# Kernel optimization log

Hardware: AMD Instinct MI355X
Metric: run time of the kernel (lower is better)

Reference implementation:

```python
import jax, jax.numpy as jnp
import numpy as np

N = 100000   # nodes
E = 1600000  # edges
G = 2048     # graphs in batch
NF = 64      # node_feature_dim
D = 32       # hidden dim (hard-coded in module)
SF = 512     # solvent_feature_dim
BN_EPS = 1e-5


def setup_inputs() -> dict:
    key = jax.random.key(0)
    ks = jax.random.split(key, 24)
    s = 0.1
    return {
        "x": jax.random.normal(ks[0], (N, NF), jnp.float32),
        "edge_index": jax.random.randint(ks[1], (2, E), 0, N, dtype=jnp.int64),
        "batch": jnp.sort(jax.random.randint(ks[2], (N,), 0, G, dtype=jnp.int64)),
        "solvent_fingerprint": jax.random.uniform(ks[3], (G, SF), jnp.float32),
        # GIN layer 1 first Linear (NF->D); layers 2-5 first Linear stacked (D->D)
        "w1a": jax.random.normal(ks[4], (NF, D), jnp.float32) * s,
        "b1a": jnp.zeros((D,), jnp.float32),
        "ws_a": jax.random.normal(ks[5], (4, D, D), jnp.float32) * s,
        "bs_a": jnp.zeros((4, D), jnp.float32),
        # second Linear of all 5 GIN MLPs
        "ws_b": jax.random.normal(ks[6], (5, D, D), jnp.float32) * s,
        "bs_b": jnp.zeros((5, D), jnp.float32),
        # BatchNorm affine params per layer
        "bn_g": jnp.ones((5, D), jnp.float32),
        "bn_b": jnp.zeros((5, D), jnp.float32),
        # dense head
        "fcg_w": jax.random.normal(ks[7], (D, 128), jnp.float32) * s,
        "fcg_b": jnp.zeros((128,), jnp.float32),
        "fs1_w": jax.random.normal(ks[8], (SF, 256), jnp.float32) * s,
        "fs1_b": jnp.zeros((256,), jnp.float32),
        "fs2_w": jax.random.normal(ks[9], (256, 128), jnp.float32) * s,
        "fs2_b": jnp.zeros((128,), jnp.float32),
        "fc1_w": jax.random.normal(ks[10], (256, 1024), jnp.float32) * s,
        "fc1_b": jnp.zeros((1024,), jnp.float32),
        "fc2_w": jax.random.normal(ks[11], (1024, 256), jnp.float32) * s,
        "fc2_b": jnp.zeros((256,), jnp.float32),
        "out_w": jax.random.normal(ks[12], (256, 1), jnp.float32) * s,
        "out_b": jnp.zeros((1,), jnp.float32),
    }


def _bn_relu(h, g, b):
    # BatchNorm1d training-mode math (biased batch variance), then ReLU
    mu = h.mean(axis=0)
    var = h.var(axis=0)
    return jax.nn.relu((h - mu) * jax.lax.rsqrt(var + BN_EPS) * g + b)


def reference(x, edge_index, batch, solvent_fingerprint,
              w1a, b1a, ws_a, bs_a, ws_b, bs_b, bn_g, bn_b,
              fcg_w, fcg_b, fs1_w, fs1_b, fs2_w, fs2_b,
              fc1_w, fc1_b, fc2_w, fc2_b, out_w, out_b):
    src, dst = edge_index[0], edge_index[1]

    def gin_agg(h):
        # GINConv with eps=0: (1+eps)*x_i + sum_{j->i} x_j
        return h + jax.ops.segment_sum(h[src], dst, num_segments=N)

    # layer 1 (NF -> D)
    h = gin_agg(x)
    h = jax.nn.relu(h @ w1a + b1a) @ ws_b[0] + bs_b[0]
    h = _bn_relu(h, bn_g[0], bn_b[0])
    # layers 2-5 (D -> D)
    for i in range(4):
        h = gin_agg(h)
        h = jax.nn.relu(h @ ws_a[i] + bs_a[i]) @ ws_b[i + 1] + bs_b[i + 1]
        h = _bn_relu(h, bn_g[i + 1], bn_b[i + 1])

    pooled = jax.ops.segment_sum(h, batch, num_segments=G)  # [G, D]
    gfeat = jax.nn.relu(pooled @ fcg_w + fcg_b)             # dropout inactive (eval)

    sf = solvent_fingerprint.reshape(-1, SF)
    s = jax.nn.relu(sf @ fs1_w + fs1_b)
    s = jax.nn.relu(s @ fs2_w + fs2_b)

    z = jnp.concatenate([gfeat, s], axis=1)                 # [G, 256]
    z = jax.nn.relu(z @ fc1_w + fc1_b)
    z = jax.nn.relu(z @ fc2_w + fc2_b)
    return z @ out_w + out_b                                # [G, 1]
```

## Files before the change

### kernel.cpp

```cpp
#include <hip/hip_runtime.h>
#include <hip/hip_bf16.h>

static constexpr int N_NODES = 100000;
static constexpr int N_EDGES = 1600000;
static constexpr int N_GRAPH = 2048;
static constexpr float BN_EPS_C = 1e-5f;

static constexpr int BUCK_SHIFT = 9;
static constexpr int NB_BUCK = (N_NODES + 511) >> 9;
static constexpr int PART_B = 256;
static constexpr int CHUNK = N_EDGES / PART_B;
static constexpr int NTOT = NB_BUCK * PART_B;
static constexpr int NSLOT = 8;

typedef unsigned int uint;
typedef unsigned short ushort;


__device__ inline uint pk2(float a, float b) {
    uint ua = __float_as_uint(a), ub = __float_as_uint(b);
    ua = (ua + 0x7fffu + ((ua >> 16) & 1u)) >> 16;
    ub = (ub + 0x7fffu + ((ub >> 16) & 1u)) >> 16;
    return ua | (ub << 16);
}
__device__ inline float b2f_lo(uint u) { return __uint_as_float(u << 16); }
__device__ inline float b2f_hi(uint u) { return __uint_as_float(u & 0xffff0000u); }

__device__ inline void unpack8(uint4 v, float* f) {
    f[0] = b2f_lo(v.x); f[1] = b2f_hi(v.x);
    f[2] = b2f_lo(v.y); f[3] = b2f_hi(v.y);
    f[4] = b2f_lo(v.z); f[5] = b2f_hi(v.z);
    f[6] = b2f_lo(v.w); f[7] = b2f_hi(v.w);
}


__global__ __launch_bounds__(256) void k_bcount(const int* __restrict__ dst, int* __restrict__ cnt) {
    __shared__ int h[NB_BUCK];
    int blk = blockIdx.x, tid = threadIdx.x;
    for (int i = tid; i < NB_BUCK; i += 256) h[i] = 0;
    __syncthreads();
    int base = blk * CHUNK;
    for (int e = base + tid; e < base + CHUNK; e += 256) {
        int d = __builtin_nontemporal_load(&dst[e]);
        atomicAdd(&h[d >> BUCK_SHIFT], 1);
    }
    __syncthreads();
    for (int i = tid; i < NB_BUCK; i += 256) cnt[i * PART_B + blk] = h[i];
}

__global__ __launch_bounds__(256) void k_scan_partial2(const int* __restrict__ v, int* __restrict__ part, int n) {
    __shared__ int sw[4];
    int b = blockIdx.x, tid = threadIdx.x;
    int base = b * 1024;
    int s = 0;
#pragma unroll
    for (int r = 0; r < 4; ++r) {
        int i = base + r * 256 + tid;
        if (i < n) s += v[i];
    }
#pragma unroll
    for (int off = 32; off > 0; off >>= 1) s += __shfl_down(s, off);
    if ((tid & 63) == 0) sw[tid >> 6] = s;
    __syncthreads();
    if (tid == 0) part[b] = sw[0] + sw[1] + sw[2] + sw[3];
}

__global__ __launch_bounds__(256) void k_scan_offsets2(int* __restrict__ part, int nb, int* __restrict__ bstart) {
    __shared__ int sh[256];
    int tid = threadIdx.x;
    sh[tid] = (tid < nb) ? part[tid] : 0;
    __syncthreads();
    if (tid == 0) {
        int run = 0;
        for (int i = 0; i < nb; ++i) { int v = sh[i]; sh[i] = run; run += v; }
        bstart[NB_BUCK] = run;
    }
    __syncthreads();
    if (tid < nb) part[tid] = sh[tid];
}

__global__ __launch_bounds__(256) void k_scan_final2(int* __restrict__ cnt, const int* __restrict__ part,
                                                     int* __restrict__ bstart, int n) {
    __shared__ int wsum[4];
    int b = blockIdx.x, tid = threadIdx.x;
    int lane = tid & 63, w = tid >> 6;
    int base = b * 1024 + tid * 4;
    int v[4];
#pragma unroll
    for (int r = 0; r < 4; ++r) {
        int i = base + r;
        v[r] = (i < n) ? cnt[i] : 0;
    }
    int tsum = v[0] + v[1] + v[2] + v[3];
    int inc = tsum;
#pragma unroll
    for (int off = 1; off < 64; off <<= 1) {
        int t = __shfl_up(inc, off);
        if (lane >= off) inc += t;
    }
    if (lane == 63) wsum[w] = inc;
    __syncthreads();
    int woff = 0;
    for (int ww = 0; ww < w; ++ww) woff += wsum[ww];
    int run = part[b] + woff + (inc - tsum);
#pragma unroll
    for (int r = 0; r < 4; ++r) {
        int idx = base + r;
        if (idx < n) {
            int c = v[r];
            cnt[idx] = run;
            if ((idx & (PART_B - 1)) == 0) bstart[idx / PART_B] = run;
            run += c;
        }
    }
}

__global__ __launch_bounds__(256) void k_bpart(const int* __restrict__ src, const int* __restrict__ dst,
                                               const int* __restrict__ cnt, int2* __restrict__ ebuf) {
    __shared__ int cur[NB_BUCK];
    int blk = blockIdx.x, tid = threadIdx.x;
    for (int i = tid; i < NB_BUCK; i += 256) cur[i] = cnt[i * PART_B + blk];
    __syncthreads();
    int base = blk * CHUNK;
    for (int e = base + tid; e < base + CHUNK; e += 256) {
        int d = __builtin_nontemporal_load(&dst[e]);
        int s = __builtin_nontemporal_load(&src[e]);
        int p = atomicAdd(&cur[d >> BUCK_SHIFT], 1);
        ebuf[p] = make_int2(d, s);
    }
}

__global__ __launch_bounds__(256) void k_bfine(const int2* __restrict__ ebuf, const int* __restrict__ bstart,
                                               int* __restrict__ row_ptr, int* __restrict__ row_end,
                                               int* __restrict__ ssrc) {
    __shared__ int fh[512];
    __shared__ int wsum[4];
    int b = blockIdx.x, tid = threadIdx.x;
    int n0 = b << BUCK_SHIFT;
    int e0 = bstart[b], e1 = bstart[b + 1];
    fh[tid] = 0; fh[tid + 256] = 0;
    __syncthreads();
    for (int e = e0 + tid; e < e1; e += 256)
        atomicAdd(&fh[ebuf[e].x - n0], 1);
    __syncthreads();
    int a0 = fh[2 * tid], a1 = fh[2 * tid + 1];
    int s = a0 + a1;
    int lane = tid & 63, w = tid >> 6;
    int inc = s;
#pragma unroll
    for (int off = 1; off < 64; off <<= 1) {
        int t = __shfl_up(inc, off);
        if (lane >= off) inc += t;
    }
    if (lane == 63) wsum[w] = inc;
    __syncthreads();
    int woff = 0;
    for (int ww = 0; ww < w; ++ww) woff += wsum[ww];
    int excl = woff + inc - s;
    int p0 = excl, p1 = excl + a0;
    int node0 = n0 + 2 * tid, node1 = node0 + 1;
    if (node0 < N_NODES) { row_ptr[node0] = e0 + p0; row_end[node0] = e0 + p0 + a0; }
    if (node1 < N_NODES) { row_ptr[node1] = e0 + p1; row_end[node1] = e0 + p1 + a1; }
    fh[2 * tid] = p0; fh[2 * tid + 1] = p1;
    __syncthreads();
    for (int e = e0 + tid; e < e1; e += 256) {
        int2 v = ebuf[e];
        int p = atomicAdd(&fh[v.x - n0], 1);
        ssrc[e0 + p] = v.y;
    }
}


__global__ __launch_bounds__(256) void k_xw1(const float* __restrict__ x, const float* __restrict__ Wa,
                                             ushort* __restrict__ y) {
    __shared__ float sWa[2048];
    int tid = threadIdx.x;
    for (int i = tid; i < 2048; i += 256) {
        int r = i >> 5, c = i & 31;
        sWa[(r << 5) + (c ^ (((r >> 4) & 3) << 2))] = Wa[i];
    }
    __syncthreads();
    int idx = blockIdx.x * 256 + tid;
    int node = idx >> 2;
    int sl = idx & 3;
    int k0 = sl * 16;
    bool active = node < N_NODES;

    float xv[16];
    if (active) {
        const float* xr = x + (size_t)node * 64 + k0;
        *(float4*)(xv + 0)  = *(const float4*)(xr + 0);
        *(float4*)(xv + 4)  = *(const float4*)(xr + 4);
        *(float4*)(xv + 8)  = *(const float4*)(xr + 8);
        *(float4*)(xv + 12) = *(const float4*)(xr + 12);
    } else {
#pragma unroll
        for (int j = 0; j < 16; ++j) xv[j] = 0.f;
    }

    float pj[32];
#pragma unroll
    for (int j = 0; j < 32; ++j) pj[j] = 0.f;
    int sw = sl << 2;
#pragma unroll
    for (int kk = 0; kk < 16; ++kk) {
        float a = xv[kk];
        const float* rb = sWa + ((k0 + kk) << 5);
#pragma unroll
        for (int j4 = 0; j4 < 8; ++j4) {
            int jo = j4 << 2;
            float4 wv = *(const float4*)(rb + (jo ^ sw));
            pj[jo + 0] = fmaf(a, wv.x, pj[jo + 0]);
            pj[jo + 1] = fmaf(a, wv.y, pj[jo + 1]);
            pj[jo + 2] = fmaf(a, wv.z, pj[jo + 2]);
            pj[jo + 3] = fmaf(a, wv.w, pj[jo + 3]);
        }
    }
#pragma unroll
    for (int j = 0; j < 32; ++j) {
        pj[j] += __shfl_xor(pj[j], 1);
        pj[j] += __shfl_xor(pj[j], 2);
    }
    if (active && sl == 0) {
        uint pk[16];
#pragma unroll
        for (int j = 0; j < 16; ++j) pk[j] = pk2(pj[2 * j], pj[2 * j + 1]);
        uint4* yp = (uint4*)(y + (size_t)node * 32);
        yp[0] = make_uint4(pk[0], pk[1], pk[2], pk[3]);
        yp[1] = make_uint4(pk[4], pk[5], pk[6], pk[7]);
        yp[2] = make_uint4(pk[8], pk[9], pk[10], pk[11]);
        yp[3] = make_uint4(pk[12], pk[13], pk[14], pk[15]);
    }
}


__global__ __launch_bounds__(256) void k_fused1y(const ushort* __restrict__ y,
                                                 const int* __restrict__ row_ptr, const int* __restrict__ row_end,
                                                 const int* __restrict__ ssrc,
                                                 const float* __restrict__ ba,
                                                 const float* __restrict__ Wb, const float* __restrict__ bb,
                                                 ushort* __restrict__ uout, float* __restrict__ stats_out) {
    __shared__ float sWb[1024];
    __shared__ float sba[32];
    __shared__ float sbb[32];
    __shared__ float bstats[64];
    __shared__ float tile[64][36];
    int tid = threadIdx.x;
    for (int i = tid; i < 1024; i += 256) sWb[i] = Wb[i];
    if (tid < 32) { sba[tid] = ba[tid]; sbb[tid] = bb[tid]; }
    if (tid < 64) bstats[tid] = 0.f;
    __syncthreads();

    int idx = blockIdx.x * 256 + tid;
    int node = idx >> 2;
    int sl = idx & 3;
    int f8 = sl * 8;
    int nloc = tid >> 2;
    bool active = node < N_NODES;

    float acc[8] = {0.f, 0.f, 0.f, 0.f, 0.f, 0.f, 0.f, 0.f};
    if (active) {
        unpack8(*(const uint4*)(y + (size_t)node * 32 + f8), acc);
        int e = row_ptr[node], e1 = row_end[node];
        float v[8];
        for (; e + 4 <= e1; e += 4) {
            int s0 = ssrc[e], s1 = ssrc[e + 1], s2 = ssrc[e + 2], s3 = ssrc[e + 3];
            uint4 va = *(const uint4*)(y + (size_t)s0 * 32 + f8);
            uint4 vb = *(const uint4*)(y + (size_t)s1 * 32 + f8);
            uint4 vc = *(const uint4*)(y + (size_t)s2 * 32 + f8);
            uint4 vd = *(const uint4*)(y + (size_t)s3 * 32 + f8);
            unpack8(va, v);
#pragma unroll
            for (int j = 0; j < 8; ++j) acc[j] += v[j];
            unpack8(vb, v);
#pragma unroll
            for (int j = 0; j < 8; ++j) acc[j] += v[j];
            unpack8(vc, v);
#pragma unroll
            for (int j = 0; j < 8; ++j) acc[j] += v[j];
            unpack8(vd, v);
#pragma unroll
            for (int j = 0; j < 8; ++j) acc[j] += v[j];
        }
        for (; e < e1; ++e) {
            int s = ssrc[e];
            unpack8(*(const uint4*)(y + (size_t)s * 32 + f8), v);
#pragma unroll
            for (int j = 0; j < 8; ++j) acc[j] += v[j];
        }
    }

    float h8[8];
#pragma unroll
    for (int j = 0; j < 8; ++j) h8[j] = fmaxf(acc[j] + sba[f8 + j], 0.f);
    *(float4*)&tile[nloc][f8] = make_float4(h8[0], h8[1], h8[2], h8[3]);
    *(float4*)&tile[nloc][f8 + 4] = make_float4(h8[4], h8[5], h8[6], h8[7]);
    __syncthreads();

    float uu[8];
#pragma unroll
    for (int j = 0; j < 8; ++j) uu[j] = sbb[f8 + j];
#pragma unroll
    for (int k4 = 0; k4 < 8; ++k4) {
        float4 hv = *(const float4*)&tile[nloc][k4 * 4];
        float hvv[4] = {hv.x, hv.y, hv.z, hv.w};
#pragma unroll
        for (int m = 0; m < 4; ++m) {
            int k = k4 * 4 + m;
            float a = hvv[m];
            const float4* wr = (const float4*)(sWb + k * 32 + f8);
            float4 w0 = wr[0], w1 = wr[1];
            uu[0] = fmaf(a, w0.x, uu[0]);
            uu[1] = fmaf(a, w0.y, uu[1]);
            uu[2] = fmaf(a, w0.z, uu[2]);
            uu[3] = fmaf(a, w0.w, uu[3]);
            uu[4] = fmaf(a, w1.x, uu[4]);
            uu[5] = fmaf(a, w1.y, uu[5]);
            uu[6] = fmaf(a, w1.z, uu[6]);
            uu[7] = fmaf(a, w1.w, uu[7]);
        }
    }

    if (active) {
        uint4 pkv = make_uint4(pk2(uu[0], uu[1]), pk2(uu[2], uu[3]), pk2(uu[4], uu[5]), pk2(uu[6], uu[7]));
        *(uint4*)(uout + (size_t)node * 32 + f8) = pkv;
    } else {
#pragma unroll
        for (int j = 0; j < 8; ++j) uu[j] = 0.f;
    }

#pragma unroll
    for (int j = 0; j < 8; ++j) {
        float v = uu[j];
        float v2 = v * v;
        v += __shfl_xor(v, 4);  v2 += __shfl_xor(v2, 4);
        v += __shfl_xor(v, 8);  v2 += __shfl_xor(v2, 8);
        v += __shfl_xor(v, 16); v2 += __shfl_xor(v2, 16);
        v += __shfl_xor(v, 32); v2 += __shfl_xor(v2, 32);
        if ((tid & 63) < 4) {
            atomicAdd(&bstats[f8 + j], v);
            atomicAdd(&bstats[32 + f8 + j], v2);
        }
    }
    __syncthreads();
    if (tid < 64) atomicAdd(&stats_out[(blockIdx.x & (NSLOT - 1)) * 64 + tid], bstats[tid]);
}


__global__ __launch_bounds__(256) void k_fused(const ushort* __restrict__ uin, ushort* __restrict__ uout,
                                               const float* __restrict__ stats_in, float* __restrict__ stats_out,
                                               const float* __restrict__ bng, const float* __restrict__ bnb,
                                               const int* __restrict__ row_ptr, const int* __restrict__ row_end,
                                               const int* __restrict__ ssrc,
                                               const float* __restrict__ Wa, const float* __restrict__ ba,
                                               const float* __restrict__ Wb, const float* __restrict__ bb) {
    __shared__ float sWa[1024];
    __shared__ float sWb[1024];
    __shared__ float sba[32];
    __shared__ float sbb[32];
    __shared__ float bstats[64];
    int tid = threadIdx.x;
    for (int i = tid; i < 1024; i += 256) {
        int r = i >> 5, c = i & 31;
        sWa[(r << 5) + (c ^ (((r >> 3) & 3) << 2))] = Wa[i];
        sWb[i] = Wb[i];
    }
    if (tid < 32) { sba[tid] = ba[tid]; sbb[tid] = bb[tid]; }
    if (tid < 64) bstats[tid] = 0.f;
    __syncthreads();

    int idx = blockIdx.x * 256 + tid;
    int node = idx >> 2;
    int sl = idx & 3;
    int f8 = sl * 8;
    bool active = node < N_NODES;

    const float inv = 1.0f / (float)N_NODES;
    float sc[8], sh[8];
    {
        float s1[8] = {0,0,0,0,0,0,0,0}, s2[8] = {0,0,0,0,0,0,0,0};
        for (int s = 0; s < NSLOT; ++s) {
            const float* sp = stats_in + s * 64;
            float4 a = *(const float4*)(sp + f8);
            float4 b = *(const float4*)(sp + f8 + 4);
            float4 c = *(const float4*)(sp + 32 + f8);
            float4 d = *(const float4*)(sp + 36 + f8);
            s1[0] += a.x; s1[1] += a.y; s1[2] += a.z; s1[3] += a.w;
            s1[4] += b.x; s1[5] += b.y; s1[6] += b.z; s1[7] += b.w;
            s2[0] += c.x; s2[1] += c.y; s2[2] += c.z; s2[3] += c.w;
            s2[4] += d.x; s2[5] += d.y; s2[6] += d.z; s2[7] += d.w;
        }
        float g[8], b[8];
        *(float4*)g = *(const float4*)(bng + f8); *(float4*)(g + 4) = *(const float4*)(bng + f8 + 4);
        *(float4*)b = *(const float4*)(bnb + f8); *(float4*)(b + 4) = *(const float4*)(bnb + f8 + 4);
#pragma unroll
        for (int j = 0; j < 8; ++j) {
            float mu = s1[j] * inv;
            sc[j] = rsqrtf(s2[j] * inv - mu * mu + BN_EPS_C) * g[j];
            sh[j] = b[j] - mu * sc[j];
        }
    }

    float acc[8] = {0.f, 0.f, 0.f, 0.f, 0.f, 0.f, 0.f, 0.f};
    if (active) {
        float v[8];
        unpack8(*(const uint4*)(uin + (size_t)node * 32 + f8), v);
#pragma unroll
        for (int j = 0; j < 8; ++j) acc[j] = fmaxf(fmaf(v[j], sc[j], sh[j]), 0.f);
        int e = row_ptr[node], e1 = row_end[node];
        for (; e + 4 <= e1; e += 4) {
            int s0 = ssrc[e], s1 = ssrc[e + 1], s2 = ssrc[e + 2], s3 = ssrc[e + 3];
            uint4 va = *(const uint4*)(uin + (size_t)s0 * 32 + f8);
            uint4 vb = *(const uint4*)(uin + (size_t)s1 * 32 + f8);
            uint4 vc = *(const uint4*)(uin + (size_t)s2 * 32 + f8);
            uint4 vd = *(const uint4*)(uin + (size_t)s3 * 32 + f8);
            unpack8(va, v);
#pragma unroll
            for (int j = 0; j < 8; ++j) acc[j] += fmaxf(fmaf(v[j], sc[j], sh[j]), 0.f);
            unpack8(vb, v);
#pragma unroll
            for (int j = 0; j < 8; ++j) acc[j] += fmaxf(fmaf(v[j], sc[j], sh[j]), 0.f);
            unpack8(vc, v);
#pragma unroll
            for (int j = 0; j < 8; ++j) acc[j] += fmaxf(fmaf(v[j], sc[j], sh[j]), 0.f);
            unpack8(vd, v);
#pragma unroll
            for (int j = 0; j < 8; ++j) acc[j] += fmaxf(fmaf(v[j], sc[j], sh[j]), 0.f);
        }
        for (; e < e1; ++e) {
            int s = ssrc[e];
            unpack8(*(const uint4*)(uin + (size_t)s * 32 + f8), v);
#pragma unroll
            for (int j = 0; j < 8; ++j) acc[j] += fmaxf(fmaf(v[j], sc[j], sh[j]), 0.f);
        }
    }

    float pj[32];
#pragma unroll
    for (int j = 0; j < 32; ++j) pj[j] = 0.f;
    int sw = sl << 2;
#pragma unroll
    for (int kk = 0; kk < 8; ++kk) {
        float a = acc[kk];
        const float* rb = sWa + ((f8 + kk) << 5);
#pragma unroll
        for (int j4 = 0; j4 < 8; ++j4) {
            int jo = j4 << 2;
            float4 wv = *(const float4*)(rb + (jo ^ sw));
            pj[jo + 0] = fmaf(a, wv.x, pj[jo + 0]);
            pj[jo + 1] = fmaf(a, wv.y, pj[jo + 1]);
            pj[jo + 2] = fmaf(a, wv.z, pj[jo + 2]);
            pj[jo + 3] = fmaf(a, wv.w, pj[jo + 3]);
        }
    }
#pragma unroll
    for (int j = 0; j < 32; ++j) {
        pj[j] += __shfl_xor(pj[j], 1);
        pj[j] += __shfl_xor(pj[j], 2);
        pj[j] = fmaxf(pj[j] + sba[j], 0.f);
    }

    float uu[8];
#pragma unroll
    for (int j = 0; j < 8; ++j) uu[j] = sbb[f8 + j];
#pragma unroll
    for (int k = 0; k < 32; ++k) {
        float a = pj[k];
        const float4* wr = (const float4*)(sWb + k * 32 + f8);
        float4 w0 = wr[0], w1 = wr[1];
        uu[0] = fmaf(a, w0.x, uu[0]);
        uu[1] = fmaf(a, w0.y, uu[1]);
        uu[2] = fmaf(a, w0.z, uu[2]);
        uu[3] = fmaf(a, w0.w, uu[3]);
        uu[4] = fmaf(a, w1.x, uu[4]);
        uu[5] = fmaf(a, w1.y, uu[5]);
        uu[6] = fmaf(a, w1.z, uu[6]);
        uu[7] = fmaf(a, w1.w, uu[7]);
    }

    if (active) {
        uint4 pkv = make_uint4(pk2(uu[0], uu[1]), pk2(uu[2], uu[3]), pk2(uu[4], uu[5]), pk2(uu[6], uu[7]));
        *(uint4*)(uout + (size_t)node * 32 + f8) = pkv;
    } else {
#pragma unroll
        for (int j = 0; j < 8; ++j) uu[j] = 0.f;
    }

#pragma unroll
    for (int j = 0; j < 8; ++j) {
        float v = uu[j];
        float v2 = v * v;
        v += __shfl_xor(v, 4);  v2 += __shfl_xor(v2, 4);
        v += __shfl_xor(v, 8);  v2 += __shfl_xor(v2, 8);
        v += __shfl_xor(v, 16); v2 += __shfl_xor(v2, 16);
        v += __shfl_xor(v, 32); v2 += __shfl_xor(v2, 32);
        if ((tid & 63) < 4) {
            atomicAdd(&bstats[f8 + j], v);
            atomicAdd(&bstats[32 + f8 + j], v2);
        }
    }
    __syncthreads();
    if (tid < 64) atomicAdd(&stats_out[(blockIdx.x & (NSLOT - 1)) * 64 + tid], bstats[tid]);
}


__global__ __launch_bounds__(256) void k_bn_pool(const ushort* __restrict__ u, const float* __restrict__ stats,
                                                 const float* __restrict__ bng, const float* __restrict__ bnb,
                                                 const int* __restrict__ batch, float* __restrict__ pooled) {
    const int CH = 128;
    int wid = (blockIdx.x * 256 + threadIdx.x) >> 6;
    int lane = threadIdx.x & 63;
    int f = lane & 31, par = lane >> 5;
    int n0 = wid * CH;
    if (n0 >= N_NODES) return;
    int n1 = n0 + CH; if (n1 > N_NODES) n1 = N_NODES;
    const float inv = 1.0f / (float)N_NODES;
    float sv = 0.f, sq = 0.f;
    for (int s = 0; s < NSLOT; ++s) { sv += stats[s * 64 + f]; sq += stats[s * 64 + 32 + f]; }
    float mu = sv * inv;
    float var = sq * inv - mu * mu;
    float sc = rsqrtf(var + BN_EPS_C) * bng[f];
    float sh = bnb[f] - mu * sc;
    float acc = 0.f;
    int curg = -1;
    for (int n = n0 + par; n < n1; n += 2) {
        int g = batch[n];
        if (g != curg) {
            if (curg >= 0) atomicAdd(&pooled[(size_t)curg * 32 + f], acc);
            acc = 0.f; curg = g;
        }
        float v = b2f_lo((uint)u[(size_t)n * 32 + f]);
        acc += fmaxf(fmaf(v, sc, sh), 0.f);
    }
    if (curg >= 0) atomicAdd(&pooled[(size_t)curg * 32 + f], acc);
}


#define GEMM_COMPUTE_16()                                                      \
    _Pragma("unroll")                                                          \
    for (int k = 0; k < 16; ++k) {                                             \
        float4 a4 = *(const float4*)&As[k][ty * 4];                            \
        float4 b4 = *(const float4*)&Bs[k][tx * 4];                            \
        acc[0][0] = fmaf(a4.x, b4.x, acc[0][0]);                               \
        acc[0][1] = fmaf(a4.x, b4.y, acc[0][1]);                               \
        acc[0][2] = fmaf(a4.x, b4.z, acc[0][2]);                               \
        acc[0][3] = fmaf(a4.x, b4.w, acc[0][3]);                               \
        acc[1][0] = fmaf(a4.y, b4.x, acc[1][0]);                               \
        acc[1][1] = fmaf(a4.y, b4.y, acc[1][1]);                               \
        acc[1][2] = fmaf(a4.y, b4.z, acc[1][2]);                               \
        acc[1][3] = fmaf(a4.y, b4.w, acc[1][3]);                               \
        acc[2][0] = fmaf(a4.z, b4.x, acc[2][0]);                               \
        acc[2][1] = fmaf(a4.z, b4.y, acc[2][1]);                               \
        acc[2][2] = fmaf(a4.z, b4.z, acc[2][2]);                               \
        acc[2][3] = fmaf(a4.z, b4.w, acc[2][3]);                               \
        acc[3][0] = fmaf(a4.w, b4.x, acc[3][0]);                               \
        acc[3][1] = fmaf(a4.w, b4.y, acc[3][1]);                               \
        acc[3][2] = fmaf(a4.w, b4.z, acc[3][2]);                               \
        acc[3][3] = fmaf(a4.w, b4.w, acc[3][3]);                               \
    }

__global__ __launch_bounds__(256) void k_gemm_f(const float* __restrict__ A, const float* __restrict__ B,
                                                const float* __restrict__ bias, float* __restrict__ C,
                                                int Nc, int K, int ldc, int do_relu) {
    __shared__ float As[16][64];
    __shared__ float Bs[16][64];
    int tid = threadIdx.x;
    int tx = tid & 15, ty = tid >> 4;
    int bm = blockIdx.x * 64, bn = blockIdx.y * 64;
    float acc[4][4] = {{0.f}};
    int am = tid >> 2;
    int ak = (tid & 3) * 4;
    int bk = tid >> 4;
    int bn4 = (tid & 15) * 4;
    const float* Ap = A + (size_t)(bm + am) * K + ak;
    const float* Bp = B + (size_t)bk * Nc + bn + bn4;
    float4 av = *(const float4*)Ap;
    float4 bv = *(const float4*)Bp;
    for (int k0 = 0; k0 < K; k0 += 16) {
        As[ak + 0][am] = av.x;
        As[ak + 1][am] = av.y;
        As[ak + 2][am] = av.z;
        As[ak + 3][am] = av.w;
        *(float4*)&Bs[bk][bn4] = bv;
        __syncthreads();
        if (k0 + 16 < K) {
            av = *(const float4*)(Ap + k0 + 16);
            bv = *(const float4*)(Bp + (size_t)(k0 + 16) * Nc);
        }
        GEMM_COMPUTE_16()
        __syncthreads();
    }
    float4 bi = *(const float4*)(bias + bn + tx * 4);
#pragma unroll
    for (int i = 0; i < 4; ++i) {
        float4 v;
        v.x = acc[i][0] + bi.x;
        v.y = acc[i][1] + bi.y;
        v.z = acc[i][2] + bi.z;
        v.w = acc[i][3] + bi.w;
        if (do_relu) {
            v.x = fmaxf(v.x, 0.f); v.y = fmaxf(v.y, 0.f);
            v.z = fmaxf(v.z, 0.f); v.w = fmaxf(v.w, 0.f);
        }
        *(float4*)(C + (size_t)(bm + ty * 4 + i) * ldc + bn + tx * 4) = v;
    }
}

__global__ __launch_bounds__(256) void k_gemm_p(const float* __restrict__ A, const float* __restrict__ B,
                                                float* __restrict__ psum, int Nc, int Ktot, int klen) {
    __shared__ float As[16][64];
    __shared__ float Bs[16][64];
    int tid = threadIdx.x;
    int tx = tid & 15, ty = tid >> 4;
    int bm = blockIdx.x * 64, bn = blockIdx.y * 64;
    int kb = blockIdx.z * klen;
    float acc[4][4] = {{0.f}};
    int am = tid >> 2;
    int ak = (tid & 3) * 4;
    int bk = tid >> 4;
    int bn4 = (tid & 15) * 4;
    const float* Ap = A + (size_t)(bm + am) * Ktot + kb + ak;
    const float* Bp = B + (size_t)(kb + bk) * Nc + bn + bn4;
    float4 av = *(const float4*)Ap;
    float4 bv = *(const float4*)Bp;
    for (int k0 = 0; k0 < klen; k0 += 16) {
        As[ak + 0][am] = av.x;
        As[ak + 1][am] = av.y;
        As[ak + 2][am] = av.z;
        As[ak + 3][am] = av.w;
        *(float4*)&Bs[bk][bn4] = bv;
        __syncthreads();
        if (k0 + 16 < klen) {
            av = *(const float4*)(Ap + k0 + 16);
            bv = *(const float4*)(Bp + (size_t)(k0 + 16) * Nc);
        }
        GEMM_COMPUTE_16()
        __syncthreads();
    }
    float* out = psum + (size_t)blockIdx.z * N_GRAPH * Nc;
#pragma unroll
    for (int i = 0; i < 4; ++i) {
        float4 v = make_float4(acc[i][0], acc[i][1], acc[i][2], acc[i][3]);
        *(float4*)(out + (size_t)(bm + ty * 4 + i) * Nc + bn + tx * 4) = v;
    }
}

__global__ __launch_bounds__(256) void k_reduce(const float* __restrict__ psum, const float* __restrict__ bias,
                                                float* __restrict__ C, int S, int Nc, int ldc, int do_relu) {
    int idx = blockIdx.x * 256 + threadIdx.x;
    int nq = Nc >> 2;
    if (idx >= N_GRAPH * nq) return;
    int m = idx / nq;
    int j = (idx - m * nq) * 4;
    float4 s = *(const float4*)(psum + (size_t)m * Nc + j);
    for (int z = 1; z < S; ++z) {
        float4 t = *(const float4*)(psum + (size_t)z * N_GRAPH * Nc + (size_t)m * Nc + j);
        s.x += t.x; s.y += t.y; s.z += t.z; s.w += t.w;
    }
    float4 bi = *(const float4*)(bias + j);
    s.x += bi.x; s.y += bi.y; s.z += bi.z; s.w += bi.w;
    if (do_relu) {
        s.x = fmaxf(s.x, 0.f); s.y = fmaxf(s.y, 0.f);
        s.z = fmaxf(s.z, 0.f); s.w = fmaxf(s.w, 0.f);
    }
    *(float4*)(C + (size_t)m * ldc + j) = s;
}


__global__ __launch_bounds__(256) void k_out(const float* __restrict__ z2, const float* __restrict__ w,
                                             const float* __restrict__ b, float* __restrict__ out) {
    int gid = blockIdx.x * 256 + threadIdx.x;
    int g = gid >> 6;
    int lane = threadIdx.x & 63;
    if (g >= N_GRAPH) return;
    float4 a = *(const float4*)(z2 + (size_t)g * 256 + lane * 4);
    float4 wv = *(const float4*)(w + lane * 4);
    float v = a.x * wv.x + a.y * wv.y + a.z * wv.z + a.w * wv.w;
#pragma unroll
    for (int off = 32; off > 0; off >>= 1) v += __shfl_down(v, off);
    if (lane == 0) out[g] = v + b[0];
}


extern "C" void kernel_launch(void* const* d_in, const int* in_sizes, int n_in,
                              void* d_out, int out_size, void* d_ws, size_t ws_size,
                              hipStream_t stream) {
    const float* x     = (const float*)d_in[0];
    const int*   eidx  = (const int*)d_in[1];
    const int*   batch = (const int*)d_in[2];
    const float* sf    = (const float*)d_in[3];
    const float* w1a   = (const float*)d_in[4];
    const float* b1a   = (const float*)d_in[5];
    const float* ws_a  = (const float*)d_in[6];
    const float* bs_a  = (const float*)d_in[7];
    const float* ws_b  = (const float*)d_in[8];
    const float* bs_b  = (const float*)d_in[9];
    const float* bn_g  = (const float*)d_in[10];
    const float* bn_b  = (const float*)d_in[11];
    const float* fcg_w = (const float*)d_in[12];
    const float* fcg_b = (const float*)d_in[13];
    const float* fs1_w = (const float*)d_in[14];
    const float* fs1_b = (const float*)d_in[15];
    const float* fs2_w = (const float*)d_in[16];
    const float* fs2_b = (const float*)d_in[17];
    const float* fc1_w = (const float*)d_in[18];
    const float* fc1_b = (const float*)d_in[19];
    const float* fc2_w = (const float*)d_in[20];
    const float* fc2_b = (const float*)d_in[21];
    const float* out_w = (const float*)d_in[22];
    const float* out_b = (const float*)d_in[23];
    float* dout = (float*)d_out;

    char* p = (char*)d_ws;
    float*  scr     = (float*)p;  p += (size_t)N_NODES * 64 * 4;
    ushort* u0      = (ushort*)p; p += (size_t)N_NODES * 32 * 2;
    ushort* u1      = (ushort*)p; p += (size_t)N_NODES * 32 * 2;
    int*    ssrc    = (int*)p;    p += (size_t)N_EDGES * 4;
    int*    row_ptr = (int*)p;    p += (size_t)N_NODES * 4;
    int*    row_end = (int*)p;    p += (size_t)N_NODES * 4;
    int*    cnt     = (int*)p;    p += (size_t)NTOT * 4;
    int*    part2   = (int*)p;    p += 512 * 4;
    int*    bstart  = (int*)p;    p += 256 * 4;
    float*  stats   = (float*)p;  p += (size_t)5 * NSLOT * 64 * 4;
    float*  pooled  = (float*)p;  p += (size_t)N_GRAPH * 32 * 4;
    ushort* ybuf    = (ushort*)p; p += (size_t)N_NODES * 32 * 2;

    int2* ebuf = (int2*)scr;

    float* zcat  = scr;
    float* z1buf = zcat + 2048 * 256;
    float* z2buf = z1buf + 2048 * 1024;
    float* s1buf = z2buf + 2048 * 256;
    float* psum  = s1buf + 2048 * 256;

    size_t zero_bytes = ((size_t)5 * NSLOT * 64 + (size_t)N_GRAPH * 32) * 4;
    hipMemsetAsync(stats, 0, zero_bytes, stream);

    const int* esrc = eidx;
    const int* edst = eidx + N_EDGES;

    const int scan_blocks = NTOT / 1024;
    k_bcount<<<PART_B, 256, 0, stream>>>(edst, cnt);
    k_scan_partial2<<<scan_blocks, 256, 0, stream>>>(cnt, part2, NTOT);
    k_scan_offsets2<<<1, 256, 0, stream>>>(part2, scan_blocks, bstart);
    k_scan_final2<<<scan_blocks, 256, 0, stream>>>(cnt, part2, bstart, NTOT);
    k_bpart<<<PART_B, 256, 0, stream>>>(esrc, edst, cnt, ebuf);
    k_bfine<<<NB_BUCK, 256, 0, stream>>>(ebuf, bstart, row_ptr, row_end, ssrc);

    const int SLOT_STRIDE = NSLOT * 64;
    const int nblk4 = (N_NODES * 4 + 255) / 256;

    k_xw1<<<nblk4, 256, 0, stream>>>(x, w1a, ybuf);
    k_fused1y<<<nblk4, 256, 0, stream>>>(ybuf, row_ptr, row_end, ssrc,
                                         b1a, ws_b, bs_b, u0, stats);

    ushort* uin = u0;
    ushort* uout = u1;
    for (int L = 1; L <= 4; ++L) {
        k_fused<<<nblk4, 256, 0, stream>>>(
            uin, uout,
            stats + (size_t)(L - 1) * SLOT_STRIDE, stats + (size_t)L * SLOT_STRIDE,
            bn_g + (L - 1) * 32, bn_b + (L - 1) * 32,
            row_ptr, row_end, ssrc,
            ws_a + (size_t)(L - 1) * 1024, bs_a + (L - 1) * 32,
            ws_b + (size_t)L * 1024, bs_b + L * 32);
        ushort* t = uin; uin = uout; uout = t;
    }

    {
        int waves = (N_NODES + 127) / 128;
        int blocks = (waves + 3) / 4;
        k_bn_pool<<<blocks, 256, 0, stream>>>(uin, stats + (size_t)4 * SLOT_STRIDE,
                                              bn_g + 128, bn_b + 128, batch, pooled);
    }

    k_gemm_f<<<dim3(32, 2), 256, 0, stream>>>(pooled, fcg_w, fcg_b, zcat, 128, 32, 256, 1);
    k_gemm_p<<<dim3(32, 4, 4), 256, 0, stream>>>(sf, fs1_w, psum, 256, 512, 128);
    k_reduce<<<512, 256, 0, stream>>>(psum, fs1_b, s1buf, 4, 256, 256, 1);
    k_gemm_p<<<dim3(32, 2, 4), 256, 0, stream>>>(s1buf, fs2_w, psum, 128, 256, 64);
    k_reduce<<<256, 256, 0, stream>>>(psum, fs2_b, zcat + 128, 4, 128, 256, 1);
    k_gemm_f<<<dim3(32, 16), 256, 0, stream>>>(zcat, fc1_w, fc1_b, z1buf, 1024, 256, 1024, 1);
    k_gemm_p<<<dim3(32, 4, 4), 256, 0, stream>>>(z1buf, fc2_w, psum, 256, 1024, 256);
    k_reduce<<<512, 256, 0, stream>>>(psum, fc2_b, z2buf, 4, 256, 256, 1);
    k_out<<<512, 256, 0, stream>>>(z2buf, out_w, out_b, dout);
}
```

Baseline: 525.0 us.

## Reorder nodes by in-degree within buckets to balance wavefront gather work

Builds, inside each 512-node bucket, a permutation that sorts nodes by in-degree using a small 64-bin histogram and scan. The fused GIN aggregation kernels then process nodes in permuted order, so nodes with similar degree share a wavefront and divergence in the edge loop drops. The cost is an extra perm lookup per node and less coalesced access to the self and output rows, since neighbouring threads now touch scattered nodes within the bucket.

```diff
diff --git a/kernel.cpp b/kernel.cpp
--- a/kernel.cpp
+++ b/kernel.cpp
@@ -132,18 +132,25 @@
 
 __global__ __launch_bounds__(256) void k_bfine(const int2* __restrict__ ebuf, const int* __restrict__ bstart,
                                                int* __restrict__ row_ptr, int* __restrict__ row_end,
-                                               int* __restrict__ ssrc) {
+                                               int* __restrict__ ssrc, int* __restrict__ perm) {
     __shared__ int fh[512];
     __shared__ int wsum[4];
+    __shared__ int dh[64];
+    __shared__ int dcur[64];
     int b = blockIdx.x, tid = threadIdx.x;
     int n0 = b << BUCK_SHIFT;
     int e0 = bstart[b], e1 = bstart[b + 1];
     fh[tid] = 0; fh[tid + 256] = 0;
+    if (tid < 64) dh[tid] = 0;
     __syncthreads();
     for (int e = e0 + tid; e < e1; e += 256)
         atomicAdd(&fh[ebuf[e].x - n0], 1);
     __syncthreads();
     int a0 = fh[2 * tid], a1 = fh[2 * tid + 1];
+    int node0 = n0 + 2 * tid, node1 = node0 + 1;
+    int b0 = a0 < 63 ? a0 : 63, b1 = a1 < 63 ? a1 : 63;
+    if (node0 < N_NODES) atomicAdd(&dh[b0], 1);
+    if (node1 < N_NODES) atomicAdd(&dh[b1], 1);
     int s = a0 + a1;
     int lane = tid & 63, w = tid >> 6;
     int inc = s;
@@ -154,15 +161,26 @@
     }
     if (lane == 63) wsum[w] = inc;
     __syncthreads();
+    if (tid < 64) {
+        int dv = dh[tid];
+        int dinc = dv;
+#pragma unroll
+        for (int off = 1; off < 64; off <<= 1) {
+            int t = __shfl_up(dinc, off);
+            if (tid >= off) dinc += t;
+        }
+        dcur[tid] = n0 + (dinc - dv);
+    }
     int woff = 0;
     for (int ww = 0; ww < w; ++ww) woff += wsum[ww];
     int excl = woff + inc - s;
     int p0 = excl, p1 = excl + a0;
-    int node0 = n0 + 2 * tid, node1 = node0 + 1;
     if (node0 < N_NODES) { row_ptr[node0] = e0 + p0; row_end[node0] = e0 + p0 + a0; }
     if (node1 < N_NODES) { row_ptr[node1] = e0 + p1; row_end[node1] = e0 + p1 + a1; }
     fh[2 * tid] = p0; fh[2 * tid + 1] = p1;
     __syncthreads();
+    if (node0 < N_NODES) { int p = atomicAdd(&dcur[b0], 1); perm[p] = node0; }
+    if (node1 < N_NODES) { int p = atomicAdd(&dcur[b1], 1); perm[p] = node1; }
     for (int e = e0 + tid; e < e1; e += 256) {
         int2 v = ebuf[e];
         int p = atomicAdd(&fh[v.x - n0], 1);
@@ -236,7 +254,7 @@
 
 __global__ __launch_bounds__(256) void k_fused1y(const ushort* __restrict__ y,
                                                  const int* __restrict__ row_ptr, const int* __restrict__ row_end,
-                                                 const int* __restrict__ ssrc,
+                                                 const int* __restrict__ ssrc, const int* __restrict__ perm,
                                                  const float* __restrict__ ba,
                                                  const float* __restrict__ Wb, const float* __restrict__ bb,
                                                  ushort* __restrict__ uout, float* __restrict__ stats_out) {
@@ -252,11 +270,12 @@
     __syncthreads();
 
     int idx = blockIdx.x * 256 + tid;
-    int node = idx >> 2;
+    int nid = idx >> 2;
     int sl = idx & 3;
     int f8 = sl * 8;
     int nloc = tid >> 2;
-    bool active = node < N_NODES;
+    bool active = nid < N_NODES;
+    int node = active ? perm[nid] : 0;
 
     float acc[8] = {0.f, 0.f, 0.f, 0.f, 0.f, 0.f, 0.f, 0.f};
     if (active) {
@@ -351,7 +370,7 @@
                                                const float* __restrict__ stats_in, float* __restrict__ stats_out,
                                                const float* __restrict__ bng, const float* __restrict__ bnb,
                                                const int* __restrict__ row_ptr, const int* __restrict__ row_end,
-                                               const int* __restrict__ ssrc,
+                                               const int* __restrict__ ssrc, const int* __restrict__ perm,
                                                const float* __restrict__ Wa, const float* __restrict__ ba,
                                                const float* __restrict__ Wb, const float* __restrict__ bb) {
     __shared__ float sWa[1024];
@@ -370,10 +389,11 @@
     __syncthreads();
 
     int idx = blockIdx.x * 256 + tid;
-    int node = idx >> 2;
+    int nid = idx >> 2;
     int sl = idx & 3;
     int f8 = sl * 8;
-    bool active = node < N_NODES;
+    bool active = nid < N_NODES;
+    int node = active ? perm[nid] : 0;
 
     const float inv = 1.0f / (float)N_NODES;
     float sc[8], sh[8];
@@ -718,6 +738,7 @@
     int*    ssrc    = (int*)p;    p += (size_t)N_EDGES * 4;
     int*    row_ptr = (int*)p;    p += (size_t)N_NODES * 4;
     int*    row_end = (int*)p;    p += (size_t)N_NODES * 4;
+    int*    permb   = (int*)p;    p += (size_t)N_NODES * 4;
     int*    cnt     = (int*)p;    p += (size_t)NTOT * 4;
     int*    part2   = (int*)p;    p += 512 * 4;
     int*    bstart  = (int*)p;    p += 256 * 4;
@@ -745,13 +766,13 @@
     k_scan_offsets2<<<1, 256, 0, stream>>>(part2, scan_blocks, bstart);
     k_scan_final2<<<scan_blocks, 256, 0, stream>>>(cnt, part2, bstart, NTOT);
     k_bpart<<<PART_B, 256, 0, stream>>>(esrc, edst, cnt, ebuf);
-    k_bfine<<<NB_BUCK, 256, 0, stream>>>(ebuf, bstart, row_ptr, row_end, ssrc);
+    k_bfine<<<NB_BUCK, 256, 0, stream>>>(ebuf, bstart, row_ptr, row_end, ssrc, permb);
 
     const int SLOT_STRIDE = NSLOT * 64;
     const int nblk4 = (N_NODES * 4 + 255) / 256;
 
     k_xw1<<<nblk4, 256, 0, stream>>>(x, w1a, ybuf);
-    k_fused1y<<<nblk4, 256, 0, stream>>>(ybuf, row_ptr, row_end, ssrc,
+    k_fused1y<<<nblk4, 256, 0, stream>>>(ybuf, row_ptr, row_end, ssrc, permb,
                                          b1a, ws_b, bs_b, u0, stats);
 
     ushort* uin = u0;
@@ -761,7 +782,7 @@
             uin, uout,
             stats + (size_t)(L - 1) * SLOT_STRIDE, stats + (size_t)L * SLOT_STRIDE,
             bn_g + (L - 1) * 32, bn_b + (L - 1) * 32,
-            row_ptr, row_end, ssrc,
+            row_ptr, row_end, ssrc, permb,
             ws_a + (size_t)(L - 1) * 1024, bs_a + (L - 1) * 32,
             ws_b + (size_t)L * 1024, bs_b + L * 32);
         ushort* t = uin; uin = uout; uout = t;
```

Result: slower. 551.8 us (+5.1%).
